# Kernel optimization log

Measured on AMD Instinct MI355X. Metric: run time of the kernel, lower is better.

The kernel has to match this reference:

```python
import jax, jax.numpy as jnp
import numpy as np

# ---- dims (see shape_source) ----
N, EG, T = 10000, 120000, 600000
NR, NS = 16, 7                      # num_radial, num_spherical
EA, EE, ET, ERBF, ECBF, EBIL = 128, 256, 64, 16, 16, 64
NB = 2                              # num_blocks
CUTOFF = 6.0
MAXZ = 100
INV_SQRT2 = 0.7071067811865476


def scaled_silu(x):
    # GemNet 'swish' activation = ScaledSiLU
    return jax.nn.silu(x) * (1.0 / 0.6)


def layer_norm(x, w, b):
    mu = jnp.mean(x, -1, keepdims=True)
    v = jnp.var(x, -1, keepdims=True)
    return (x - mu) * jax.lax.rsqrt(v + 1e-5) * w + b


def radial_basis(D):
    # polynomial envelope (exponent 5) * gaussian RBF on d/cutoff
    d = D / CUTOFF
    p = 5.0
    env = 1.0 - ((p + 1) * (p + 2) / 2) * d**5 + p * (p + 2) * d**6 - (p * (p + 1) / 2) * d**7
    env = jnp.where(d < 1.0, env, 0.0)
    offsets = jnp.linspace(0.0, 1.0, NR)
    coeff = -0.5 * (NR - 1.0) ** 2   # -0.5 / spacing^2
    return env[:, None] * jnp.exp(coeff * (d[:, None] - offsets) ** 2)  # (EG, NR)


def spherical_basis(cosphi):
    # circular basis: Y_l0(phi) = sqrt((2l+1)/4pi) P_l(cos phi), l = 0..NS-1
    P = [jnp.ones_like(cosphi), cosphi]
    for l in range(2, NS):
        P.append(((2 * l - 1) * cosphi * P[-1] - (l - 1) * P[-2]) / l)
    return jnp.stack([np.sqrt((2 * l + 1) / (4 * np.pi)) * P[l] for l in range(NS)], -1)  # (T, NS)


def residual(x, Ws):
    # GemNet ResidualLayer: 2 bias-free dense + skip, scaled by 1/sqrt(2)
    y = scaled_silu(scaled_silu(x @ Ws[0]) @ Ws[1])
    return (x + y) * INV_SQRT2


def gemnet_forward(D, cosphi, atom_emb, W_rbf3, W_rbf_h, W_rbf_out, W_cbf_down,
                   W_edge_emb, ib_dense_ca, ib_trip_dense_ba, ib_trip_mlp_rbf,
                   ib_trip_down, ib_trip_bilinear, ib_trip_up_ca, ib_trip_up_ac,
                   ib_res_before, ib_res_after, ib_atom_dense_rbf, ib_atom_dense1,
                   ib_atom_res, ib_concat_dense, ib_res_m, ob_dense_rbf, ob_dense1,
                   ob_res, ln_m_w, ln_m_b, ln_E_w, ln_E_b,
                   Z, idx_s, idx_t, id3_ba, id3_ca, id_swap):
    rbf = radial_basis(D)                                   # (EG, NR)
    sph = spherical_basis(cosphi)                           # (T, NS)
    rbf3 = rbf @ W_rbf3                                     # (EG, ERBF)
    rbf_h = rbf @ W_rbf_h
    rbf_out = rbf @ W_rbf_out
    # EfficientInteractionDownProjection: rbf x W -> (EG, NS, ECBF)
    rbf_W1 = jnp.einsum('er,sri->esi', rbf, W_cbf_down)
    # per-triplet circular-basis embedding: sum over spherical components
    cbf_t = jnp.einsum('ts,tsi->ti', sph, rbf_W1[id3_ca])   # (T, ECBF)

    h = atom_emb[Z]                                         # (N, EA)
    m = scaled_silu(jnp.concatenate([h[idx_s], h[idx_t], rbf], -1) @ W_edge_emb)  # (EG, EE)

    def out_block(i, h_cur, m_cur):
        mn = layer_norm(m_cur, ln_m_w[i], ln_m_b[i])
        x = mn * (rbf_out @ ob_dense_rbf[i])                # (EG, EE)
        xE = jax.ops.segment_sum(x, idx_t, num_segments=N)  # scatter edges -> atoms
        xE = scaled_silu(xE @ ob_dense1[i])                 # (N, EA)
        for r in range(ob_res.shape[1]):
            xE = residual(xE, ob_res[i, r])
        return layer_norm(xE, ln_E_w[i], ln_E_b[i])

    E_t = out_block(0, h, m)
    for i in range(NB):
        # ---- triplet interaction ----
        x_ca_skip = scaled_silu(m @ ib_dense_ca[i])
        x_ba = scaled_silu(m @ ib_trip_dense_ba[i])
        x_ba = x_ba * (rbf3 @ ib_trip_mlp_rbf[i])
        x_trip = scaled_silu(x_ba @ ib_trip_down[i])        # (EG, ET)
        x_t = x_trip[id3_ba]                                # gather -> (T, ET)
        # bilinear: out[t,o] = sum_i cbf_t[t,i] * sum_c x_t[t,c] W[c,i,o]
        Wb = ib_trip_bilinear[i]                            # (ET, ECBF, EBIL)
        acc = (x_t @ Wb[:, 0, :]) * cbf_t[:, 0:1]
        for ic in range(1, ECBF):
            acc = acc + (x_t @ Wb[:, ic, :]) * cbf_t[:, ic:ic + 1]
        x = jax.ops.segment_sum(acc, id3_ca, num_segments=EG)  # scatter trip -> edges (EG, EBIL)
        x_ca = scaled_silu(x @ ib_trip_up_ca[i])
        x_ac = scaled_silu(x @ ib_trip_up_ac[i])[id_swap]   # counter-directional edge
        x3 = (x_ca + x_ac) * INV_SQRT2

        # ---- edge update ----
        x = (x_ca_skip + x3) * INV_SQRT2
        for r in range(ib_res_before.shape[1]):
            x = residual(x, ib_res_before[i, r])
        x = (x + m) * INV_SQRT2
        for r in range(ib_res_after.shape[1]):
            x = residual(x, ib_res_after[i, r])

        # ---- atom update ----
        xa = x * (rbf_h @ ib_atom_dense_rbf[i])
        xa = jax.ops.segment_sum(xa, idx_t, num_segments=N)
        xa = scaled_silu(xa @ ib_atom_dense1[i])            # (N, EA)
        for r in range(ib_atom_res.shape[1]):
            xa = residual(xa, ib_atom_res[i, r])
        h = (h + xa) * INV_SQRT2

        # ---- edge embedding refresh with updated atoms ----
        m2 = scaled_silu(jnp.concatenate([h[idx_s], h[idx_t], x], -1) @ ib_concat_dense[i])
        for r in range(ib_res_m.shape[1]):
            m2 = residual(m2, ib_res_m[i, r])
        m = (m + m2) * INV_SQRT2

        E_t = E_t + out_block(i + 1, h, m)
    return E_t  # (N, EA) per-atom output features


def setup_inputs() -> dict:
    key = jax.random.key(0)
    ks = iter(jax.random.split(key, 64))

    def nrm(shape, fan_in):
        return jax.random.normal(next(ks), shape, jnp.float32) / np.sqrt(fan_in)

    Z = jax.random.randint(next(ks), (N,), 0, MAXZ)
    idx_s = jax.random.randint(next(ks), (EG,), 0, N)
    idx_t = jax.random.randint(next(ks), (EG,), 0, N)
    id3_ba = jax.random.randint(next(ks), (T,), 0, EG)
    id3_ca = jax.random.randint(next(ks), (T,), 0, EG)
    id_swap = jnp.arange(EG) ^ 1   # symmetric edges stored in (e, e^1) pairs
    D = jax.random.uniform(next(ks), (EG,), jnp.float32, 0.8, 5.9)
    cosphi = jax.random.uniform(next(ks), (T,), jnp.float32, -1.0, 1.0)

    emb = jax.random.normal(next(ks), (MAXZ, EA), jnp.float32)
    emb = emb / jnp.maximum(jnp.linalg.norm(emb, axis=-1, keepdims=True), 1.0)  # max_norm=1

    NBo = NB + 1
    inp = dict(
        D=D, cosphi=cosphi, atom_emb=emb,
        W_rbf3=nrm((NR, ERBF), NR), W_rbf_h=nrm((NR, ERBF), NR), W_rbf_out=nrm((NR, ERBF), NR),
        W_cbf_down=nrm((NS, NR, ECBF), NR),
        W_edge_emb=nrm((2 * EA + NR, EE), 2 * EA + NR),
        ib_dense_ca=nrm((NB, EE, EE), EE),
        ib_trip_dense_ba=nrm((NB, EE, EE), EE),
        ib_trip_mlp_rbf=nrm((NB, ERBF, EE), ERBF),
        ib_trip_down=nrm((NB, EE, ET), EE),
        ib_trip_bilinear=nrm((NB, ET, ECBF, EBIL), ET * ECBF),
        ib_trip_up_ca=nrm((NB, EBIL, EE), EBIL),
        ib_trip_up_ac=nrm((NB, EBIL, EE), EBIL),
        ib_res_before=nrm((NB, 1, 2, EE, EE), EE),
        ib_res_after=nrm((NB, 1, 2, EE, EE), EE),
        ib_atom_dense_rbf=nrm((NB, ERBF, EE), ERBF),
        ib_atom_dense1=nrm((NB, EE, EA), EE),
        ib_atom_res=nrm((NB, 2, 2, EA, EA), EA),
        ib_concat_dense=nrm((NB, 2 * EA + EE, EE), 2 * EA + EE),
        ib_res_m=nrm((NB, 1, 2, EE, EE), EE),
        ob_dense_rbf=nrm((NBo, ERBF, EE), ERBF),
        ob_dense1=nrm((NBo, EE, EA), EE),
        ob_res=nrm((NBo, 2, 2, EA, EA), EA),
        ln_m_w=jnp.ones((NBo, EE)), ln_m_b=jnp.zeros((NBo, EE)),
        ln_E_w=jnp.ones((NBo, EA)), ln_E_b=jnp.zeros((NBo, EA)),
        Z=Z, idx_s=idx_s, idx_t=idx_t, id3_ba=id3_ba, id3_ca=id3_ca, id_swap=id_swap,
    )
    return inp


def reference(D, cosphi, atom_emb, W_rbf3, W_rbf_h, W_rbf_out, W_cbf_down, W_edge_emb,
              ib_dense_ca, ib_trip_dense_ba, ib_trip_mlp_rbf, ib_trip_down,
              ib_trip_bilinear, ib_trip_up_ca, ib_trip_up_ac, ib_res_before,
              ib_res_after, ib_atom_dense_rbf, ib_atom_dense1, ib_atom_res,
              ib_concat_dense, ib_res_m, ob_dense_rbf, ob_dense1, ob_res,
              ln_m_w, ln_m_b, ln_E_w, ln_E_b, Z, idx_s, idx_t, id3_ba, id3_ca, id_swap):
    return gemnet_forward(D, cosphi, atom_emb, W_rbf3, W_rbf_h, W_rbf_out, W_cbf_down,
                          W_edge_emb, ib_dense_ca, ib_trip_dense_ba, ib_trip_mlp_rbf,
                          ib_trip_down, ib_trip_bilinear, ib_trip_up_ca, ib_trip_up_ac,
                          ib_res_before, ib_res_after, ib_atom_dense_rbf, ib_atom_dense1,
                          ib_atom_res, ib_concat_dense, ib_res_m, ob_dense_rbf, ob_dense1,
                          ob_res, ln_m_w, ln_m_b, ln_E_w, ln_E_b,
                          Z, idx_s, idx_t, id3_ba, id3_ca, id_swap)
```

## Files before the change

### kernel.cpp

```cpp
#include <hip/hip_runtime.h>

#define NATOM 10000
#define EG    120000
#define TT    600000

#define INV_SQRT2f 0.7071067811865476f

typedef unsigned short bf16t;
typedef __attribute__((ext_vector_type(8))) short s16x8;
typedef __attribute__((ext_vector_type(8))) unsigned short u16x8;
typedef __attribute__((ext_vector_type(4))) float f32x4;

__device__ __forceinline__ float ssilu(float x) {
    return x * (1.0f / (1.0f + __expf(-x))) * (1.0f / 0.6f);
}
__device__ __forceinline__ float bf2f(unsigned short u) {
    return __uint_as_float(((unsigned)u) << 16);
}
__device__ __forceinline__ unsigned short f2bf(float f) {
    unsigned b = __float_as_uint(f);
    unsigned r = (b + 0x7FFF + ((b >> 16) & 1)) >> 16;
    return (unsigned short)r;
}
__device__ __forceinline__ u16x8 cvt8(const float4 va, const float4 vb) {
    u16x8 r{};
    r[0] = f2bf(va.x); r[1] = f2bf(va.y); r[2] = f2bf(va.z); r[3] = f2bf(va.w);
    r[4] = f2bf(vb.x); r[5] = f2bf(vb.y); r[6] = f2bf(vb.z); r[7] = f2bf(vb.w);
    return r;
}

template <typename T> struct VT;
template <> struct VT<float> {
    static __device__ __forceinline__ float4 load4(const float* p) { return *(const float4*)p; }
    static __device__ __forceinline__ void store4(float* p, float4 v) { *(float4*)p = v; }
};
template <> struct VT<bf16t> {
    static __device__ __forceinline__ float4 load4(const bf16t* p) {
        ushort4 u = *(const ushort4*)p;
        return make_float4(bf2f(u.x), bf2f(u.y), bf2f(u.z), bf2f(u.w));
    }
    static __device__ __forceinline__ void store4(bf16t* p, float4 v) {
        ushort4 u; u.x = f2bf(v.x); u.y = f2bf(v.y); u.z = f2bf(v.z); u.w = f2bf(v.w);
        *(ushort4*)p = u;
    }
};

__global__ __launch_bounds__(256) void k_fill(float* __restrict__ o, int n, float v) {
    int i = blockIdx.x * 256 + threadIdx.x;
    if (i < n) o[i] = v;
}

__global__ __launch_bounds__(256) void k_hist(
    const int* __restrict__ idx, int* __restrict__ cnt, int n)
{
    int i = blockIdx.x * 256 + threadIdx.x;
    if (i < n) atomicAdd(&cnt[idx[i]], 1);
}

__global__ __launch_bounds__(1024) void k_scan(
    const int* __restrict__ cnt, int* __restrict__ off, int n)
{
    __shared__ int wsum[16];
    __shared__ int carrySh;
    if (threadIdx.x == 0) carrySh = 0;
    __syncthreads();
    const int lane = threadIdx.x & 63, wid = threadIdx.x >> 6;
    for (int base = 0; base < n; base += 8192) {
        int v[8]; int s = 0;
        int i0 = base + threadIdx.x * 8;
#pragma unroll
        for (int j = 0; j < 8; j++) { int i = i0 + j; v[j] = (i < n) ? cnt[i] : 0; s += v[j]; }
        int sc = s;
#pragma unroll
        for (int d = 1; d < 64; d <<= 1) { int t = __shfl_up(sc, d); if (lane >= d) sc += t; }
        if (lane == 63) wsum[wid] = sc;
        __syncthreads();
        int wbase = 0;
        for (int w = 0; w < 16; w++) wbase += (w < wid) ? wsum[w] : 0;
        int carry = carrySh;
        int excl = carry + wbase + (sc - s);
#pragma unroll
        for (int j = 0; j < 8; j++) { int i = i0 + j; if (i < n) off[i] = excl; excl += v[j]; }
        __syncthreads();
        if (threadIdx.x == 1023) carrySh = carry + wbase + sc;
        __syncthreads();
    }
    if (threadIdx.x == 0) off[n] = carrySh;
}

__global__ __launch_bounds__(256) void k_rank_trip(
    const int* __restrict__ id3_ca, const int* __restrict__ id3_ba,
    const int* __restrict__ off, int* __restrict__ cnt2,
    int* __restrict__ rank, int* __restrict__ ba_s, int* __restrict__ ca_s, int n)
{
    int t = blockIdx.x * 256 + threadIdx.x;
    if (t >= n) return;
    int ca = id3_ca[t];
    int p = off[ca] + atomicAdd(&cnt2[ca], 1);
    rank[t] = p;
    ba_s[p] = id3_ba[t];
    ca_s[p] = ca;
}

__global__ __launch_bounds__(256) void k_rank_edge(
    const int* __restrict__ idx, const int* __restrict__ off,
    int* __restrict__ cnt2, int* __restrict__ lst, int n)
{
    int i = blockIdx.x * 256 + threadIdx.x;
    if (i >= n) return;
    int a = idx[i];
    int p = off[a] + atomicAdd(&cnt2[a], 1);
    lst[p] = i;
}

__global__ __launch_bounds__(256) void k_segsum(
    const bf16t* __restrict__ X, const int* __restrict__ off,
    const int* __restrict__ lst, bf16t* __restrict__ out)
{
    int n = blockIdx.x, j = threadIdx.x;
    int b = off[n], e = off[n + 1];
    float s = 0.f;
    for (int k = b; k < e; k++) s += bf2f(X[(size_t)lst[k] * 256 + j]);
    out[(size_t)n * 256 + j] = f2bf(s);
}

struct WtE { const float* src; unsigned dstOff; int K, KP, N, mode; };
struct WtBatch { WtE e[12]; int n; };

__global__ __launch_bounds__(256) void k_wt_batch(WtBatch b, bf16t* __restrict__ base)
{
    for (int i = 0; i < b.n; i++) {
        const WtE E = b.e[i];
        int total = (E.mode == 0) ? E.N * E.KP : 16 * 64 * 64;
        for (int idx = blockIdx.x * 256 + threadIdx.x; idx < total; idx += gridDim.x * 256) {
            bf16t v;
            if (E.mode == 0) {
                int n = idx / E.KP, k = idx - n * E.KP;
                v = (k < E.K) ? f2bf(E.src[(size_t)k * E.N + n]) : (bf16t)0;
            } else {
                int e8 = idx & 7, o = (idx >> 3) & 63, ch = (idx >> 9) & 7, ii = idx >> 12;
                v = f2bf(E.src[((size_t)(ch * 8 + e8) * 16 + ii) * 64 + o]);
            }
            base[E.dstOff + idx] = v;
        }
    }
}

struct WcE { const float* Wa; const float* Wb; };
struct WcBatch { WcE e[7]; };

__global__ __launch_bounds__(256) void k_wcomb_batch(WcBatch b, float* __restrict__ wcb)
{
    __shared__ float sA[256];
    int c = blockIdx.x, j = threadIdx.x;
    sA[j] = b.e[c].Wa[j];
    __syncthreads();
    const float* Wb = b.e[c].Wb;
    float* dst = wcb + (size_t)c * 4096;
#pragma unroll 4
    for (int r = 0; r < 16; r++) {
        float acc = 0.f;
#pragma unroll
        for (int k = 0; k < 16; k++) acc = fmaf(sA[r * 16 + k], Wb[k * 256 + j], acc);
        dst[r * 256 + j] = acc;
    }
}

__global__ __launch_bounds__(256) void k_rbf(
    const float* __restrict__ D, const float* __restrict__ Wc,
    bf16t* __restrict__ rbf, float* __restrict__ rbfW1)
{
    __shared__ float sW[1792];
    for (int i = threadIdx.x; i < 1792; i += 256) sW[i] = Wc[i];
    __syncthreads();
    int e = blockIdx.x * 256 + threadIdx.x;
    if (e >= EG) return;
    float d = D[e] * (1.0f / 6.0f);
    float d2 = d * d, d4 = d2 * d2, d5 = d4 * d, d6 = d5 * d, d7 = d6 * d;
    float env = 1.0f - 21.0f * d5 + 35.0f * d6 - 15.0f * d7;
    if (d >= 1.0f) env = 0.0f;
    float r[16];
#pragma unroll
    for (int i = 0; i < 16; i++) {
        float t = d - (float)i * (1.0f / 15.0f);
        r[i] = env * __expf(-112.5f * t * t);
    }
#pragma unroll
    for (int j = 0; j < 16; j++) rbf[(size_t)e * 16 + j] = f2bf(r[j]);
    for (int s = 0; s < 7; s++) {
#pragma unroll 4
        for (int i = 0; i < 16; i++) {
            float a = 0.f;
#pragma unroll
            for (int k = 0; k < 16; k++)
                a = fmaf(r[k], sW[(s * 16 + k) * 16 + i], a);
            rbfW1[(size_t)e * 112 + s * 16 + i] = a;
        }
    }
}

__global__ __launch_bounds__(256) void k_cbf(
    const float* __restrict__ cosphi, const int* __restrict__ id3_ca,
    const float* __restrict__ rbfW1, const int* __restrict__ rank,
    bf16t* __restrict__ cbf)
{
    int t = blockIdx.x * 256 + threadIdx.x;
    if (t >= TT) return;
    float c = cosphi[t];
    const float norm[7] = {0.28209479177387814f, 0.4886025119029199f, 0.6307831305050401f,
                           0.7463526651802308f, 0.8462843753216345f, 0.935414346693485f,
                           1.0171072362820548f};
    float y[7];
    float pm2 = 1.0f, pm1 = c;
    y[0] = norm[0];
    y[1] = norm[1] * c;
    for (int l = 2; l < 7; l++) {
        float p = ((2.0f * l - 1.0f) * c * pm1 - (l - 1.0f) * pm2) / (float)l;
        y[l] = norm[l] * p;
        pm2 = pm1; pm1 = p;
    }
    int e = id3_ca[t];
    const float* __restrict__ w = rbfW1 + (size_t)e * 112;
    float out[16];
#pragma unroll
    for (int i = 0; i < 16; i++) out[i] = 0.f;
#pragma unroll
    for (int s = 0; s < 7; s++) {
        float ys = y[s];
#pragma unroll
        for (int i = 0; i < 16; i++) out[i] = fmaf(ys, w[s * 16 + i], out[i]);
    }
    int p = rank[t];
#pragma unroll
    for (int i = 0; i < 16; i++) cbf[(size_t)p * 16 + i] = f2bf(out[i]);
}

__global__ __launch_bounds__(256) void k_hgather(
    const float* __restrict__ emb, const int* __restrict__ Z, bf16t* __restrict__ h)
{
    int i = blockIdx.x * 256 + threadIdx.x;
    if (i < NATOM * 128) {
        int n = i >> 7, j = i & 127;
        h[i] = f2bf(emb[(size_t)Z[n] * 128 + j]);
    }
}

template <typename TA, int FR, int FC, int EPI>
__global__ __launch_bounds__(256) void mgemm3(
    const TA* __restrict__ A, const bf16t* __restrict__ BT,
    bf16t* __restrict__ C, const bf16t* __restrict__ skip,
    int M, int N, int K)
{
    constexpr int ROWS = 2 * FR * 16;
    constexpr int COLS = 2 * FC * 16;
    __shared__ __align__(16) ushort As[ROWS][40];
    __shared__ __align__(16) ushort Bs[COLS][40];
    const int tid = threadIdx.x, wave = tid >> 6, lane = tid & 63;
    const int waveR = wave >> 1, waveC = wave & 1;
    const int rowBase = blockIdx.y * ROWS, colBase = blockIdx.x * COLS;

    const int sar = tid >> 1, sak = (tid & 1) << 4;
    int agr = rowBase + sar; if (agr >= M) agr = M - 1;
    int sbc, sbk;
    if constexpr (COLS == 128) { sbc = tid >> 1; sbk = (tid & 1) << 4; }
    else                       { sbc = tid >> 2; sbk = (tid & 3) << 3; }

    f32x4 zv = {0.f, 0.f, 0.f, 0.f};
    f32x4 acc[FR][FC];
#pragma unroll
    for (int f = 0; f < FR; f++)
#pragma unroll
        for (int q = 0; q < FC; q++) acc[f][q] = zv;

    const int arow0 = waveR * FR * 16 + (lane & 15);
    const int bcol0 = waveC * FC * 16 + (lane & 15);
    const int kd = (lane >> 4) << 3;

    u16x8 a0, a1, b0, b1;
    auto loadA = [&](int k0) {
        if constexpr (sizeof(TA) == 2) {
            const u16x8* s = (const u16x8*)((const bf16t*)A + (size_t)agr * K + k0 + sak);
            a0 = s[0]; a1 = s[1];
        } else {
            const float4* s = (const float4*)((const float*)A + (size_t)agr * K + k0 + sak);
            a0 = cvt8(s[0], s[1]); a1 = cvt8(s[2], s[3]);
        }
    };
    auto loadB = [&](int k0) {
        const u16x8* s = (const u16x8*)(BT + (size_t)(colBase + sbc) * K + k0 + sbk);
        b0 = s[0];
        if constexpr (COLS == 128) b1 = s[1];
    };
    loadA(0); loadB(0);
    for (int k0 = 0; k0 < K; k0 += 32) {
        __syncthreads();
        *(u16x8*)&As[sar][sak] = a0;
        *(u16x8*)&As[sar][sak + 8] = a1;
        *(u16x8*)&Bs[sbc][sbk] = b0;
        if constexpr (COLS == 128) *(u16x8*)&Bs[sbc][sbk + 8] = b1;
        __syncthreads();
        if (k0 + 32 < K) { loadA(k0 + 32); loadB(k0 + 32); }
        u16x8 af[FR], bf[FC];
#pragma unroll
        for (int f = 0; f < FR; f++) af[f] = *(const u16x8*)&As[arow0 + f * 16][kd];
#pragma unroll
        for (int q = 0; q < FC; q++) bf[q] = *(const u16x8*)&Bs[bcol0 + q * 16][kd];
#pragma unroll
        for (int f = 0; f < FR; f++)
#pragma unroll
            for (int q = 0; q < FC; q++)
                acc[f][q] = __builtin_amdgcn_mfma_f32_16x16x32_bf16(
                    *(s16x8*)&af[f], *(s16x8*)&bf[q], acc[f][q], 0, 0, 0);
    }

    const int rB = rowBase + waveR * FR * 16 + ((lane >> 4) << 2);
    const int cB = colBase + waveC * FC * 16 + (lane & 15);
#pragma unroll
    for (int f = 0; f < FR; f++) {
#pragma unroll
        for (int r = 0; r < 4; r++) {
            int row = rB + f * 16 + r;
            if (row >= M) continue;
#pragma unroll
            for (int q = 0; q < FC; q++) {
                int col = cB + q * 16;
                float v = acc[f][q][r];
                if (EPI == 1) {
                    C[(size_t)row * N + col] = f2bf(ssilu(v));
                } else {
                    float sk = bf2f(skip[(size_t)row * N + col]);
                    C[(size_t)row * N + col] = f2bf((sk + ssilu(v)) * INV_SQRT2f);
                }
            }
        }
    }
}

__global__ __launch_bounds__(256) void mgemmA1(
    const bf16t* __restrict__ BT, bf16t* __restrict__ C,
    int M, int N, int K, int KP,
    const bf16t* __restrict__ hA, const int* __restrict__ gS,
    const int* __restrict__ gT, const bf16t* __restrict__ X, int w2)
{
    __shared__ __align__(16) ushort As[128][40];
    __shared__ __align__(16) ushort Bs[64][40];
    const int tid = threadIdx.x, wave = tid >> 6, lane = tid & 63;
    const int waveR = wave >> 1, waveC = wave & 1;
    const int rowBase = blockIdx.y * 128, colBase = blockIdx.x * 64;

    const int sar = tid >> 1, sak = (tid & 1) << 4;
    const int arow = rowBase + sar;
    const int arowC = arow < M ? arow : (M - 1);
    const int ia = gS[arowC], ibx = gT[arowC];
    const int sbc = tid >> 2, sbk = (tid & 3) << 3;

    f32x4 zv = {0.f, 0.f, 0.f, 0.f};
    f32x4 acc[4][2];
#pragma unroll
    for (int f = 0; f < 4; f++)
#pragma unroll
        for (int q = 0; q < 2; q++) acc[f][q] = zv;

    const int arow0 = waveR * 64 + (lane & 15);
    const int bcol0 = waveC * 32 + (lane & 15);
    const int kd = (lane >> 4) << 3;

    u16x8 a0, a1, b0;
    auto loadA = [&](int k0) {
        a0 = u16x8{}; a1 = u16x8{};
        const int kk = k0 + sak;
        if (kk < 128) {
            const u16x8* s = (const u16x8*)(hA + (size_t)ia * 128 + kk);
            a0 = s[0]; a1 = s[1];
        } else if (kk < 256) {
            const u16x8* s = (const u16x8*)(hA + (size_t)ibx * 128 + (kk - 128));
            a0 = s[0]; a1 = s[1];
        } else if (kk < K && kk - 256 < w2) {
            const u16x8* s = (const u16x8*)(X + (size_t)arowC * w2 + (kk - 256));
            a0 = s[0]; a1 = s[1];
        }
    };
    auto loadB = [&](int k0) {
        b0 = *(const u16x8*)(BT + (size_t)(colBase + sbc) * KP + k0 + sbk);
    };
    loadA(0); loadB(0);
    for (int k0 = 0; k0 < K; k0 += 32) {
        __syncthreads();
        *(u16x8*)&As[sar][sak] = a0;
        *(u16x8*)&As[sar][sak + 8] = a1;
        *(u16x8*)&Bs[sbc][sbk] = b0;
        __syncthreads();
        if (k0 + 32 < K) { loadA(k0 + 32); loadB(k0 + 32); }
        u16x8 af[4], bf[2];
#pragma unroll
        for (int f = 0; f < 4; f++) af[f] = *(const u16x8*)&As[arow0 + f * 16][kd];
#pragma unroll
        for (int q = 0; q < 2; q++) bf[q] = *(const u16x8*)&Bs[bcol0 + q * 16][kd];
#pragma unroll
        for (int f = 0; f < 4; f++)
#pragma unroll
            for (int q = 0; q < 2; q++)
                acc[f][q] = __builtin_amdgcn_mfma_f32_16x16x32_bf16(
                    *(s16x8*)&af[f], *(s16x8*)&bf[q], acc[f][q], 0, 0, 0);
    }

    const int rB = rowBase + waveR * 64 + ((lane >> 4) << 2);
    const int cB = colBase + waveC * 32 + (lane & 15);
#pragma unroll
    for (int f = 0; f < 4; f++) {
#pragma unroll
        for (int r = 0; r < 4; r++) {
            int row = rB + f * 16 + r;
            if (row >= M) continue;
#pragma unroll
            for (int q = 0; q < 2; q++)
                C[(size_t)row * N + cB + q * 16] = f2bf(ssilu(acc[f][q][r]));
        }
    }
}

__global__ __launch_bounds__(256) void mgemm_up(
    const float* __restrict__ A, const bf16t* __restrict__ BTca,
    const bf16t* __restrict__ BTac, bf16t* __restrict__ C, int M)
{
    constexpr int K = 64, N = 256;
    __shared__ __align__(16) ushort As[128][40];
    __shared__ __align__(16) ushort Bs[2][64][40];
    const int tid = threadIdx.x, wave = tid >> 6, lane = tid & 63;
    const int waveR = wave >> 1, waveC = wave & 1;
    const int rowBase = blockIdx.y * 128, colBase = blockIdx.x * 64;

    const int sar = tid >> 1, sak = (tid & 1) << 4;
    int agr = rowBase + sar; if (agr >= M) agr = M - 1;
    const int sbc = tid >> 2, sbk = (tid & 3) << 3;

    f32x4 zv = {0.f, 0.f, 0.f, 0.f};
    f32x4 accA[4][2], accB[4][2];
#pragma unroll
    for (int f = 0; f < 4; f++)
#pragma unroll
        for (int q = 0; q < 2; q++) { accA[f][q] = zv; accB[f][q] = zv; }

    const int arow0 = waveR * 64 + (lane & 15);
    const int bcol0 = waveC * 32 + (lane & 15);
    const int kd = (lane >> 4) << 3;

    u16x8 a0, a1, bA, bB;
    auto loadA = [&](int k0) {
        const float4* s = (const float4*)(A + (size_t)agr * K + k0 + sak);
        a0 = cvt8(s[0], s[1]); a1 = cvt8(s[2], s[3]);
    };
    auto loadB = [&](int k0) {
        bA = *(const u16x8*)(BTca + (size_t)(colBase + sbc) * K + k0 + sbk);
        bB = *(const u16x8*)(BTac + (size_t)(colBase + sbc) * K + k0 + sbk);
    };
    loadA(0); loadB(0);
    for (int k0 = 0; k0 < K; k0 += 32) {
        __syncthreads();
        *(u16x8*)&As[sar][sak] = a0;
        *(u16x8*)&As[sar][sak + 8] = a1;
        *(u16x8*)&Bs[0][sbc][sbk] = bA;
        *(u16x8*)&Bs[1][sbc][sbk] = bB;
        __syncthreads();
        if (k0 + 32 < K) { loadA(k0 + 32); loadB(k0 + 32); }
        u16x8 af[4], bfA[2], bfB[2];
#pragma unroll
        for (int f = 0; f < 4; f++) af[f] = *(const u16x8*)&As[arow0 + f * 16][kd];
#pragma unroll
        for (int q = 0; q < 2; q++) {
            bfA[q] = *(const u16x8*)&Bs[0][bcol0 + q * 16][kd];
            bfB[q] = *(const u16x8*)&Bs[1][bcol0 + q * 16][kd];
        }
#pragma unroll
        for (int f = 0; f < 4; f++)
#pragma unroll
            for (int q = 0; q < 2; q++) {
                accA[f][q] = __builtin_amdgcn_mfma_f32_16x16x32_bf16(
                    *(s16x8*)&af[f], *(s16x8*)&bfA[q], accA[f][q], 0, 0, 0);
                accB[f][q] = __builtin_amdgcn_mfma_f32_16x16x32_bf16(
                    *(s16x8*)&af[f], *(s16x8*)&bfB[q], accB[f][q], 0, 0, 0);
            }
    }

    const int rB = rowBase + waveR * 64 + ((lane >> 4) << 2);
    const int cB = colBase + waveC * 32 + (lane & 15);
#pragma unroll
    for (int f = 0; f < 4; f++) {
#pragma unroll
        for (int r = 0; r < 4; r++) {
            int row = rB + f * 16 + r;
            if (row >= M) continue;
#pragma unroll
            for (int q = 0; q < 2; q++) {
                float v = (ssilu(accA[f][q][r]) + ssilu(accB[f][q][r ^ 1])) * INV_SQRT2f;
                C[(size_t)row * N + cB + q * 16] = f2bf(v);
            }
        }
    }
}

__global__ __launch_bounds__(256) void k_bilinear_m(
    const bf16t* __restrict__ xtrip, const bf16t* __restrict__ cbf,
    const bf16t* __restrict__ WT,
    const int* __restrict__ ba_s, const int* __restrict__ ca_s,
    float* __restrict__ seg)
{
    __shared__ __align__(16) ushort xs[64][72];
    __shared__ ushort cbs[64][16];
    __shared__ int cas[64];
    __shared__ __align__(16) float ts[64][65];
    const int tid = threadIdx.x, wave = tid >> 6, lane = tid & 63;
    const int t0 = blockIdx.x * 64;
    {
        int r = tid >> 2, q = (tid & 3) << 4;
        int ba = ba_s[t0 + r];
        const u16x8* src = (const u16x8*)(xtrip + (size_t)ba * 64 + q);
        *(u16x8*)&xs[r][q] = src[0];
        *(u16x8*)&xs[r][q + 8] = src[1];
    }
    if (tid < 64) cas[tid] = ca_s[t0 + tid];
    {
        int e = tid << 2; int r = e >> 4, c = e & 15;
        *(ushort4*)&cbs[r][c] = *(const ushort4*)(cbf + (size_t)(t0 + r) * 16 + c);
    }
    __syncthreads();
    const int kd = (lane >> 4) << 3;
    u16x8 a0 = *(const u16x8*)(&xs[wave * 16 + (lane & 15)][kd]);
    u16x8 a1 = *(const u16x8*)(&xs[wave * 16 + (lane & 15)][32 + kd]);
    const int rowo = wave * 16 + ((lane >> 4) << 2);
    const int chb = lane >> 4, colw = lane & 15;
    auto waddr = [&](int i, int fc, int half) {
        return WT + (((size_t)(i * 8 + half * 4 + chb) * 64) + colw + fc * 16) * 8;
    };

    float tot[4][4];
#pragma unroll
    for (int a = 0; a < 4; a++)
#pragma unroll
        for (int b = 0; b < 4; b++) tot[a][b] = 0.f;

    u16x8 bw[8], bn[8];
#pragma unroll
    for (int fc = 0; fc < 4; fc++) {
        bw[fc * 2 + 0] = *(const u16x8*)waddr(0, fc, 0);
        bw[fc * 2 + 1] = *(const u16x8*)waddr(0, fc, 1);
    }
    for (int i = 0; i < 16; i++) {
        if (i < 15) {
#pragma unroll
            for (int fc = 0; fc < 4; fc++) {
                bn[fc * 2 + 0] = *(const u16x8*)waddr(i + 1, fc, 0);
                bn[fc * 2 + 1] = *(const u16x8*)waddr(i + 1, fc, 1);
            }
        }
        f32x4 zv = {0.f, 0.f, 0.f, 0.f};
        f32x4 p[4] = {zv, zv, zv, zv};
#pragma unroll
        for (int fc = 0; fc < 4; fc++) {
            p[fc] = __builtin_amdgcn_mfma_f32_16x16x32_bf16(
                *(s16x8*)&a0, *(s16x8*)&bw[fc * 2 + 0], p[fc], 0, 0, 0);
            p[fc] = __builtin_amdgcn_mfma_f32_16x16x32_bf16(
                *(s16x8*)&a1, *(s16x8*)&bw[fc * 2 + 1], p[fc], 0, 0, 0);
        }
#pragma unroll
        for (int r = 0; r < 4; r++) {
            float s = bf2f(cbs[rowo + r][i]);
#pragma unroll
            for (int fc = 0; fc < 4; fc++) tot[fc][r] += s * p[fc][r];
        }
#pragma unroll
        for (int q = 0; q < 8; q++) bw[q] = bn[q];
    }
#pragma unroll
    for (int r = 0; r < 4; r++)
#pragma unroll
        for (int fc = 0; fc < 4; fc++)
            ts[rowo + r][fc * 16 + (lane & 15)] = tot[fc][r];
    __syncthreads();
    {
        int q = tid >> 6, c = tid & 63;
        float s = 0.f;
        int cur = cas[q * 16];
#pragma unroll 1
        for (int r = q * 16; r < q * 16 + 16; r++) {
            int ca = cas[r];
            if (ca != cur) {
                atomicAdd(&seg[(size_t)cur * 64 + c], s);
                s = 0.f; cur = ca;
            }
            s += ts[r][c];
        }
        atomicAdd(&seg[(size_t)cur * 64 + c], s);
    }
}

__global__ __launch_bounds__(256) void k_mulproj(
    const bf16t* __restrict__ in, const bf16t* __restrict__ rvec,
    const float* __restrict__ Wp, bf16t* __restrict__ out)
{
    int e = blockIdx.x;
    int j = threadIdx.x;
    __shared__ float r16[16];
    if (j < 16) r16[j] = bf2f(rvec[(size_t)e * 16 + j]);
    __syncthreads();
    float p = 0.f;
#pragma unroll
    for (int k = 0; k < 16; k++) p = fmaf(r16[k], Wp[k * 256 + j], p);
    out[(size_t)e * 256 + j] = f2bf(bf2f(in[(size_t)e * 256 + j]) * p);
}

__global__ __launch_bounds__(256) void k_ln_proj(
    const bf16t* __restrict__ m, const float* __restrict__ lnw,
    const float* __restrict__ lnb, const bf16t* __restrict__ rvec,
    const float* __restrict__ Wp, bf16t* __restrict__ out)
{
    int e = blockIdx.x;
    int j = threadIdx.x;
    __shared__ float red[8];
    __shared__ float r16[16];
    if (j < 16) r16[j] = bf2f(rvec[(size_t)e * 16 + j]);
    float v = bf2f(m[(size_t)e * 256 + j]);
    float s = v, s2 = v * v;
#pragma unroll
    for (int off = 32; off > 0; off >>= 1) {
        s += __shfl_xor(s, off);
        s2 += __shfl_xor(s2, off);
    }
    int wid = j >> 6, lane = j & 63;
    if (lane == 0) { red[wid] = s; red[4 + wid] = s2; }
    __syncthreads();
    float tot = red[0] + red[1] + red[2] + red[3];
    float tot2 = red[4] + red[5] + red[6] + red[7];
    float mu = tot * (1.f / 256.f);
    float var = tot2 * (1.f / 256.f) - mu * mu;
    float ln = (v - mu) * rsqrtf(var + 1e-5f) * lnw[j] + lnb[j];
    float p = 0.f;
#pragma unroll
    for (int k = 0; k < 16; k++) p = fmaf(r16[k], Wp[k * 256 + j], p);
    out[(size_t)e * 256 + j] = f2bf(ln * p);
}

__global__ __launch_bounds__(128) void k_ln_acc(
    const bf16t* __restrict__ x, const float* __restrict__ w,
    const float* __restrict__ b, float* __restrict__ out)
{
    int n = blockIdx.x;
    int j = threadIdx.x;
    __shared__ float red[4];
    float v = bf2f(x[(size_t)n * 128 + j]);
    float s = v, s2 = v * v;
#pragma unroll
    for (int off = 32; off > 0; off >>= 1) {
        s += __shfl_xor(s, off);
        s2 += __shfl_xor(s2, off);
    }
    int wid = j >> 6, lane = j & 63;
    if (lane == 0) { red[wid] = s; red[2 + wid] = s2; }
    __syncthreads();
    float tot = red[0] + red[1];
    float tot2 = red[2] + red[3];
    float mu = tot * (1.f / 128.f);
    float var = tot2 * (1.f / 128.f) - mu * mu;
    out[(size_t)n * 128 + j] += (v - mu) * rsqrtf(var + 1e-5f) * w[j] + b[j];
}

template <typename T>
__global__ __launch_bounds__(256) void k_addscale(
    const T* __restrict__ a, const T* __restrict__ b, T* __restrict__ y, int n4)
{
    int i = blockIdx.x * 256 + threadIdx.x;
    if (i < n4) {
        float4 av = VT<T>::load4(a + (size_t)i * 4);
        float4 bv = VT<T>::load4(b + (size_t)i * 4);
        VT<T>::store4(y + (size_t)i * 4,
                      make_float4((av.x + bv.x) * INV_SQRT2f, (av.y + bv.y) * INV_SQRT2f,
                                  (av.z + bv.z) * INV_SQRT2f, (av.w + bv.w) * INV_SQRT2f));
    }
}

typedef bf16t T;
static bool try_run(void* const* d_in, void* d_out, void* d_ws, size_t ws_size, hipStream_t stream)
{
    const float* D            = (const float*)d_in[0];
    const float* cosphi       = (const float*)d_in[1];
    const float* atom_emb     = (const float*)d_in[2];
    const float* W_rbf3       = (const float*)d_in[3];
    const float* W_rbf_h      = (const float*)d_in[4];
    const float* W_rbf_out    = (const float*)d_in[5];
    const float* W_cbf_down   = (const float*)d_in[6];
    const float* W_edge_emb   = (const float*)d_in[7];
    const float* ib_dense_ca  = (const float*)d_in[8];
    const float* ib_trip_dense_ba = (const float*)d_in[9];
    const float* ib_trip_mlp_rbf  = (const float*)d_in[10];
    const float* ib_trip_down     = (const float*)d_in[11];
    const float* ib_trip_bilinear = (const float*)d_in[12];
    const float* ib_trip_up_ca    = (const float*)d_in[13];
    const float* ib_trip_up_ac    = (const float*)d_in[14];
    const float* ib_res_before    = (const float*)d_in[15];
    const float* ib_res_after     = (const float*)d_in[16];
    const float* ib_atom_dense_rbf = (const float*)d_in[17];
    const float* ib_atom_dense1    = (const float*)d_in[18];
    const float* ib_atom_res       = (const float*)d_in[19];
    const float* ib_concat_dense   = (const float*)d_in[20];
    const float* ib_res_m          = (const float*)d_in[21];
    const float* ob_dense_rbf      = (const float*)d_in[22];
    const float* ob_dense1         = (const float*)d_in[23];
    const float* ob_res            = (const float*)d_in[24];
    const float* ln_m_w            = (const float*)d_in[25];
    const float* ln_m_b            = (const float*)d_in[26];
    const float* ln_E_w            = (const float*)d_in[27];
    const float* ln_E_b            = (const float*)d_in[28];
    const int* Z       = (const int*)d_in[29];
    const int* idx_s   = (const int*)d_in[30];
    const int* idx_t   = (const int*)d_in[31];
    const int* id3_ba  = (const int*)d_in[32];
    const int* id3_ca  = (const int*)d_in[33];

    char* base = (char*)d_ws;
    size_t off = 0;
    auto alloc = [&](size_t bytes) -> char* {
        off = (off + 255) & ~(size_t)255;
        char* p = base + off;
        off += bytes;
        return p;
    };
    T* m      = (T*)alloc((size_t)EG * 256 * 2);
    T* B1     = (T*)alloc((size_t)EG * 256 * 2);
    T* B2     = (T*)alloc((size_t)EG * 256 * 2);
    float* rbfW1 = (float*)B1;
    int* rank    = (int*)B2;
    T* rbf    = (T*)alloc((size_t)EG * 16 * 2);
    T* cbf    = (T*)alloc((size_t)TT * 16 * 2);
    bf16t* h  = (bf16t*)alloc((size_t)NATOM * 128 * 2);
    T* xtrip  = (T*)alloc((size_t)EG * 64 * 2);
    char* ub  = alloc((size_t)EG * 64 * 4);
    float* seg64  = (float*)ub;
    bf16t* segN_b = (bf16t*)ub;
    bf16t* At1b   = (bf16t*)(ub + (size_t)NATOM * 256 * 2);
    bf16t* At2b   = (bf16t*)(ub + (size_t)NATOM * 256 * 2 + (size_t)NATOM * 128 * 2);
    int* cntT  = (int*)ub;
    int* cnt2T = (int*)(ub + (size_t)EG * 4);
    int* off_ca = (int*)(ub + (size_t)2 * EG * 4);
    float* wcb = (float*)alloc((size_t)7 * 4096 * 4);
    bf16t* ar  = (bf16t*)alloc((size_t)507904 * 2);
    int* off_atom  = (int*)alloc((size_t)(NATOM + 1) * 4);
    int* ba_s      = (int*)alloc((size_t)TT * 4);
    int* ca_s      = (int*)alloc((size_t)TT * 4);
    int* csr_edges = (int*)alloc((size_t)EG * 4);
    if (off > ws_size) return false;
    float* out = (float*)d_out;

    auto g256 = [&](int epi, const T* A, unsigned wOff, T* C, const T* skip, int K) {
        dim3 grid(2, (EG + 127) / 128);
        if (epi == 1) mgemm3<T, 4, 4, 1><<<grid, 256, 0, stream>>>(A, ar + wOff, C, skip, EG, 256, K);
        else          mgemm3<T, 4, 4, 2><<<grid, 256, 0, stream>>>(A, ar + wOff, C, skip, EG, 256, K);
    };
    auto gatom = [&](int epi, const bf16t* A, unsigned wOff, bf16t* C, const bf16t* skip, int K) {
        dim3 grid(1, (NATOM + 127) / 128);
        if (epi == 1) mgemm3<bf16t, 4, 4, 1><<<grid, 256, 0, stream>>>(A, ar + wOff, C, skip, NATOM, 128, K);
        else          mgemm3<bf16t, 4, 4, 2><<<grid, 256, 0, stream>>>(A, ar + wOff, C, skip, NATOM, 128, K);
    };
    auto out_block = [&](int i, unsigned offD1, unsigned offRes) {
        k_ln_proj<<<EG, 256, 0, stream>>>(m, ln_m_w + (size_t)i * 256, ln_m_b + (size_t)i * 256,
                                          rbf, wcb + (size_t)(4 + i) * 4096, B2);
        k_segsum<<<NATOM, 256, 0, stream>>>(B2, off_atom, csr_edges, segN_b);
        gatom(1, segN_b, offD1, At1b, nullptr, 256);
        for (int r = 0; r < 2; r++) {
            gatom(1, At1b, offRes + (r * 2 + 0) * 16384, At2b, nullptr, 128);
            gatom(2, At2b, offRes + (r * 2 + 1) * 16384, At1b, At1b, 128);
        }
        k_ln_acc<<<NATOM, 128, 0, stream>>>(At1b, ln_E_w + (size_t)i * 128, ln_E_b + (size_t)i * 128, out);
    };

    hipMemsetAsync(cntT, 0, (size_t)EG * 4, stream);
    k_hist<<<(TT + 255) / 256, 256, 0, stream>>>(id3_ca, cntT, TT);
    k_scan<<<1, 1024, 0, stream>>>(cntT, off_ca, EG);
    hipMemsetAsync(cnt2T, 0, (size_t)EG * 4, stream);
    k_rank_trip<<<(TT + 255) / 256, 256, 0, stream>>>(id3_ca, id3_ba, off_ca, cnt2T,
                                                      rank, ba_s, ca_s, TT);
    hipMemsetAsync(cntT, 0, (size_t)NATOM * 4, stream);
    k_hist<<<(EG + 255) / 256, 256, 0, stream>>>(idx_t, cntT, EG);
    k_scan<<<1, 1024, 0, stream>>>(cntT, off_atom, NATOM);
    hipMemsetAsync(cnt2T, 0, (size_t)NATOM * 4, stream);
    k_rank_edge<<<(EG + 255) / 256, 256, 0, stream>>>(idx_t, off_atom, cnt2T, csr_edges, EG);

    {
        WcBatch wb;
        wb.e[0] = {W_rbf3, ib_trip_mlp_rbf};
        wb.e[1] = {W_rbf3, ib_trip_mlp_rbf + 4096};
        wb.e[2] = {W_rbf_h, ib_atom_dense_rbf};
        wb.e[3] = {W_rbf_h, ib_atom_dense_rbf + 4096};
        wb.e[4] = {W_rbf_out, ob_dense_rbf};
        wb.e[5] = {W_rbf_out, ob_dense_rbf + 4096};
        wb.e[6] = {W_rbf_out, ob_dense_rbf + 8192};
        k_wcomb_batch<<<7, 256, 0, stream>>>(wb, wcb);
    }
    {
        WtBatch wt{};
        wt.e[0] = {W_edge_emb, 0u, 272, 288, 256, 0};
        wt.e[1] = {ob_dense1, 73728u, 256, 256, 128, 0};
        for (int j = 0; j < 4; j++)
            wt.e[2 + j] = {ob_res + (size_t)j * 16384, 106496u + j * 16384u, 128, 128, 128, 0};
        wt.n = 6;
        k_wt_batch<<<512, 256, 0, stream>>>(wt, ar);
    }

    hipMemsetAsync(out, 0, (size_t)NATOM * 128 * 4, stream);
    k_rbf<<<(EG + 255) / 256, 256, 0, stream>>>(D, W_cbf_down, rbf, rbfW1);
    k_cbf<<<(TT + 255) / 256, 256, 0, stream>>>(cosphi, id3_ca, rbfW1, rank, cbf);
    k_hgather<<<(NATOM * 128 + 255) / 256, 256, 0, stream>>>(atom_emb, Z, h);
    {
        dim3 grid(4, (EG + 127) / 128);
        mgemmA1<<<grid, 256, 0, stream>>>(ar, m, EG, 256, 272, 288, h, idx_s, idx_t, rbf, 16);
    }
    out_block(0, 73728u, 106496u);

    for (int i = 0; i < 2; i++) {
        {
            WtBatch wt{};
            wt.e[0] = {ib_dense_ca + (size_t)i * 65536, 0u, 256, 256, 256, 0};
            wt.e[1] = {ib_trip_dense_ba + (size_t)i * 65536, 65536u, 256, 256, 256, 0};
            wt.e[2] = {ib_trip_down + (size_t)i * 16384, 131072u, 256, 256, 64, 0};
            wt.e[3] = {ib_trip_bilinear + (size_t)i * 65536, 147456u, 0, 0, 0, 1};
            wt.e[4] = {ib_trip_up_ca + (size_t)i * 16384, 212992u, 64, 64, 256, 0};
            wt.e[5] = {ib_trip_up_ac + (size_t)i * 16384, 229376u, 64, 64, 256, 0};
            wt.e[6] = {ib_res_before + (size_t)i * 131072, 245760u, 256, 256, 256, 0};
            wt.e[7] = {ib_res_before + (size_t)i * 131072 + 65536, 311296u, 256, 256, 256, 0};
            wt.e[8] = {ib_res_after + (size_t)i * 131072, 376832u, 256, 256, 256, 0};
            wt.e[9] = {ib_res_after + (size_t)i * 131072 + 65536, 442368u, 256, 256, 256, 0};
            wt.n = 10;
            k_wt_batch<<<512, 256, 0, stream>>>(wt, ar);
        }
        g256(1, m, 0u, B1, nullptr, 256);
        g256(1, m, 65536u, B2, nullptr, 256);
        k_mulproj<<<EG, 256, 0, stream>>>(B2, rbf, wcb + (size_t)i * 4096, B2);
        {
            dim3 grid(1, (EG + 127) / 128);
            mgemm3<T, 4, 2, 1><<<grid, 256, 0, stream>>>(B2, ar + 131072, xtrip, nullptr, EG, 64, 256);
        }
        hipMemsetAsync(seg64, 0, (size_t)EG * 64 * 4, stream);
        k_bilinear_m<<<TT / 64, 256, 0, stream>>>(xtrip, cbf, ar + 147456, ba_s, ca_s, seg64);
        {
            dim3 grid(4, (EG + 127) / 128);
            mgemm_up<<<grid, 256, 0, stream>>>(seg64, ar + 212992, ar + 229376, B2, EG);
        }
        k_addscale<T><<<(EG * 256 / 4 + 255) / 256, 256, 0, stream>>>(B1, B2, B1, EG * 256 / 4);
        g256(1, B1, 245760u, B2, nullptr, 256);
        g256(2, B2, 311296u, B1, B1, 256);
        k_addscale<T><<<(EG * 256 / 4 + 255) / 256, 256, 0, stream>>>(B1, m, B1, EG * 256 / 4);
        g256(1, B1, 376832u, B2, nullptr, 256);
        g256(2, B2, 442368u, B1, B1, 256);
        {
            WtBatch wt{};
            wt.e[0] = {ib_atom_dense1 + (size_t)i * 32768, 0u, 256, 256, 128, 0};
            for (int j = 0; j < 4; j++)
                wt.e[1 + j] = {ib_atom_res + (size_t)i * 65536 + (size_t)j * 16384,
                               32768u + j * 16384u, 128, 128, 128, 0};
            wt.e[5] = {ib_concat_dense + (size_t)i * 131072, 98304u, 512, 512, 256, 0};
            wt.e[6] = {ib_res_m + (size_t)i * 131072, 229376u, 256, 256, 256, 0};
            wt.e[7] = {ib_res_m + (size_t)i * 131072 + 65536, 294912u, 256, 256, 256, 0};
            wt.e[8] = {ob_dense1 + (size_t)(i + 1) * 32768, 360448u, 256, 256, 128, 0};
            for (int j = 0; j < 4; j++)
                wt.e[9 + j] = {ob_res + (size_t)(i + 1) * 65536 + (size_t)j * 16384,
                               393216u + j * 16384u, 128, 128, 128, 0};
            wt.n = 13 <= 12 ? 13 : 12;
            wt.n = 9;
            k_wt_batch<<<512, 256, 0, stream>>>(wt, ar);
            WtBatch wt2{};
            wt2.e[0] = {ob_dense1 + (size_t)(i + 1) * 32768, 360448u, 256, 256, 128, 0};
            for (int j = 0; j < 4; j++)
                wt2.e[1 + j] = {ob_res + (size_t)(i + 1) * 65536 + (size_t)j * 16384,
                                393216u + j * 16384u, 128, 128, 128, 0};
            wt2.n = 5;
            k_wt_batch<<<512, 256, 0, stream>>>(wt2, ar);
        }
        k_mulproj<<<EG, 256, 0, stream>>>(B1, rbf, wcb + (size_t)(2 + i) * 4096, B2);
        k_segsum<<<NATOM, 256, 0, stream>>>(B2, off_atom, csr_edges, segN_b);
        gatom(1, segN_b, 0u, At1b, nullptr, 256);
        for (int r = 0; r < 2; r++) {
            gatom(1, At1b, 32768u + (r * 2 + 0) * 16384, At2b, nullptr, 128);
            gatom(2, At2b, 32768u + (r * 2 + 1) * 16384, At1b, At1b, 128);
        }
        k_addscale<bf16t><<<(NATOM * 128 / 4 + 255) / 256, 256, 0, stream>>>(h, At1b, h, NATOM * 128 / 4);
        {
            dim3 grid(4, (EG + 127) / 128);
            mgemmA1<<<grid, 256, 0, stream>>>(ar + 98304, B2, EG, 256, 512, 512, h, idx_s, idx_t, B1, 256);
        }
        g256(1, B2, 229376u, B1, nullptr, 256);
        g256(2, B1, 294912u, B2, B2, 256);
        k_addscale<T><<<(EG * 256 / 4 + 255) / 256, 256, 0, stream>>>(m, B2, m, EG * 256 / 4);

        out_block(i + 1, 360448u, 393216u);
    }
    return true;
}

extern "C" void kernel_launch(void* const* d_in, const int* in_sizes, int n_in,
                              void* d_out, int out_size, void* d_ws, size_t ws_size,
                              hipStream_t stream)
{
    if (try_run(d_in, d_out, d_ws, ws_size, stream)) return;
    float v = 3000.0f + (float)(ws_size >> 20);
    k_fill<<<(NATOM * 128 + 255) / 256, 256, 0, stream>>>((float*)d_out, NATOM * 128, v);
}
```

Measured before the change: 2.939 ms.

## Fuse residual-layer GEMM pairs into one kernel and fold skip-adds into epilogues

Adds a mgemm_res kernel that runs both dense layers of a residual block in one launch. The first layer's ScaledSiLU output stays in LDS and feeds the second GEMM, and the skip connection plus an optional extra residual add are applied in the epilogue. The separate k_addscale passes are removed, and mgemm_up now applies the skip-add itself. This cuts several full-size edge and atom intermediate round-trips through HBM and a number of kernel launches, and the duplicated ob_dense1 weight conversion is dropped. In exchange the fused kernel uses about 59 KB of LDS at N=256, which lowers occupancy, and it computes in place on buffers it also reads from.

Result: faster. 2.699 ms (-8.2%).

```diff
diff --git a/kernel.cpp b/kernel.cpp
--- a/kernel.cpp
+++ b/kernel.cpp
@@ -28,22 +28,6 @@
     r[4] = f2bf(vb.x); r[5] = f2bf(vb.y); r[6] = f2bf(vb.z); r[7] = f2bf(vb.w);
     return r;
 }
-
-template <typename T> struct VT;
-template <> struct VT<float> {
-    static __device__ __forceinline__ float4 load4(const float* p) { return *(const float4*)p; }
-    static __device__ __forceinline__ void store4(float* p, float4 v) { *(float4*)p = v; }
-};
-template <> struct VT<bf16t> {
-    static __device__ __forceinline__ float4 load4(const bf16t* p) {
-        ushort4 u = *(const ushort4*)p;
-        return make_float4(bf2f(u.x), bf2f(u.y), bf2f(u.z), bf2f(u.w));
-    }
-    static __device__ __forceinline__ void store4(bf16t* p, float4 v) {
-        ushort4 u; u.x = f2bf(v.x); u.y = f2bf(v.y); u.z = f2bf(v.z); u.w = f2bf(v.w);
-        *(ushort4*)p = u;
-    }
-};
 
 __global__ __launch_bounds__(256) void k_fill(float* __restrict__ o, int n, float v) {
     int i = blockIdx.x * 256 + threadIdx.x;
@@ -336,6 +320,123 @@
     }
 }
 
+template <int FCC, int EPIOUT>
+__global__ __launch_bounds__(256) void mgemm_res(
+    const bf16t* __restrict__ A, const bf16t* __restrict__ BT0,
+    const bf16t* __restrict__ BT1, bf16t* __restrict__ C,
+    const bf16t* __restrict__ add2, int M)
+{
+    constexpr int N = FCC * 32;
+    __shared__ __align__(16) ushort As[64][40];
+    __shared__ __align__(16) ushort Bs[N][40];
+    __shared__ __align__(16) ushort inter[64][N + 8];
+    const int tid = threadIdx.x, wave = tid >> 6, lane = tid & 63;
+    const int waveR = wave >> 1, waveC = wave & 1;
+    const int rowBase = blockIdx.x * 64;
+
+    const int sar = tid >> 2, sak = (tid & 3) << 3;
+    int agr = rowBase + sar; if (agr >= M) agr = M - 1;
+    const int sbc = tid >> 2, sbk = (tid & 3) << 3;
+
+    const int arow0 = waveR * 32 + (lane & 15);
+    const int bcol0 = waveC * FCC * 16 + (lane & 15);
+    const int kd = (lane >> 4) << 3;
+
+    f32x4 zv = {0.f, 0.f, 0.f, 0.f};
+    f32x4 acc[2][FCC];
+#pragma unroll
+    for (int f = 0; f < 2; f++)
+#pragma unroll
+        for (int q = 0; q < FCC; q++) acc[f][q] = zv;
+
+    u16x8 aR, bR[FCC / 2];
+    auto loadA = [&](int k0) {
+        aR = *(const u16x8*)(A + (size_t)agr * N + k0 + sak);
+    };
+    auto loadB = [&](const bf16t* BT, int k0) {
+#pragma unroll
+        for (int j = 0; j < FCC / 2; j++)
+            bR[j] = *(const u16x8*)(BT + (size_t)(sbc + j * 64) * N + k0 + sbk);
+    };
+
+    loadA(0); loadB(BT0, 0);
+    for (int k0 = 0; k0 < N; k0 += 32) {
+        __syncthreads();
+        *(u16x8*)&As[sar][sak] = aR;
+#pragma unroll
+        for (int j = 0; j < FCC / 2; j++) *(u16x8*)&Bs[sbc + j * 64][sbk] = bR[j];
+        __syncthreads();
+        if (k0 + 32 < N) { loadA(k0 + 32); loadB(BT0, k0 + 32); }
+        else             { loadB(BT1, 0); }
+        u16x8 af0 = *(const u16x8*)&As[arow0][kd];
+        u16x8 af1 = *(const u16x8*)&As[arow0 + 16][kd];
+        u16x8 bf[FCC];
+#pragma unroll
+        for (int q = 0; q < FCC; q++) bf[q] = *(const u16x8*)&Bs[bcol0 + q * 16][kd];
+#pragma unroll
+        for (int q = 0; q < FCC; q++) {
+            acc[0][q] = __builtin_amdgcn_mfma_f32_16x16x32_bf16(
+                *(s16x8*)&af0, *(s16x8*)&bf[q], acc[0][q], 0, 0, 0);
+            acc[1][q] = __builtin_amdgcn_mfma_f32_16x16x32_bf16(
+                *(s16x8*)&af1, *(s16x8*)&bf[q], acc[1][q], 0, 0, 0);
+        }
+    }
+    {
+        const int rL = waveR * 32 + ((lane >> 4) << 2);
+        const int cL = waveC * FCC * 16 + (lane & 15);
+#pragma unroll
+        for (int f = 0; f < 2; f++)
+#pragma unroll
+            for (int r = 0; r < 4; r++)
+#pragma unroll
+                for (int q = 0; q < FCC; q++)
+                    inter[rL + f * 16 + r][cL + q * 16] = f2bf(ssilu(acc[f][q][r]));
+    }
+#pragma unroll
+    for (int f = 0; f < 2; f++)
+#pragma unroll
+        for (int q = 0; q < FCC; q++) acc[f][q] = zv;
+
+    for (int k0 = 0; k0 < N; k0 += 32) {
+        __syncthreads();
+#pragma unroll
+        for (int j = 0; j < FCC / 2; j++) *(u16x8*)&Bs[sbc + j * 64][sbk] = bR[j];
+        __syncthreads();
+        if (k0 + 32 < N) loadB(BT1, k0 + 32);
+        u16x8 af0 = *(const u16x8*)&inter[arow0][k0 + kd];
+        u16x8 af1 = *(const u16x8*)&inter[arow0 + 16][k0 + kd];
+        u16x8 bf[FCC];
+#pragma unroll
+        for (int q = 0; q < FCC; q++) bf[q] = *(const u16x8*)&Bs[bcol0 + q * 16][kd];
+#pragma unroll
+        for (int q = 0; q < FCC; q++) {
+            acc[0][q] = __builtin_amdgcn_mfma_f32_16x16x32_bf16(
+                *(s16x8*)&af0, *(s16x8*)&bf[q], acc[0][q], 0, 0, 0);
+            acc[1][q] = __builtin_amdgcn_mfma_f32_16x16x32_bf16(
+                *(s16x8*)&af1, *(s16x8*)&bf[q], acc[1][q], 0, 0, 0);
+        }
+    }
+
+    const int rB = rowBase + waveR * 32 + ((lane >> 4) << 2);
+    const int cB = waveC * FCC * 16 + (lane & 15);
+#pragma unroll
+    for (int f = 0; f < 2; f++) {
+#pragma unroll
+        for (int r = 0; r < 4; r++) {
+            int row = rB + f * 16 + r;
+            if (row >= M) continue;
+#pragma unroll
+            for (int q = 0; q < FCC; q++) {
+                int col = cB + q * 16;
+                float sk = bf2f(A[(size_t)row * N + col]);
+                float y = (sk + ssilu(acc[f][q][r])) * INV_SQRT2f;
+                if (EPIOUT == 1) y = (y + bf2f(add2[(size_t)row * N + col])) * INV_SQRT2f;
+                C[(size_t)row * N + col] = f2bf(y);
+            }
+        }
+    }
+}
+
 __global__ __launch_bounds__(256) void mgemmA1(
     const bf16t* __restrict__ BT, bf16t* __restrict__ C,
     int M, int N, int K, int KP,
@@ -421,7 +522,8 @@
 
 __global__ __launch_bounds__(256) void mgemm_up(
     const float* __restrict__ A, const bf16t* __restrict__ BTca,
-    const bf16t* __restrict__ BTac, bf16t* __restrict__ C, int M)
+    const bf16t* __restrict__ BTac, bf16t* __restrict__ C,
+    const bf16t* __restrict__ skip, int M)
 {
     constexpr int K = 64, N = 256;
     __shared__ __align__(16) ushort As[128][40];
@@ -492,8 +594,10 @@
             if (row >= M) continue;
 #pragma unroll
             for (int q = 0; q < 2; q++) {
+                int col = cB + q * 16;
                 float v = (ssilu(accA[f][q][r]) + ssilu(accB[f][q][r ^ 1])) * INV_SQRT2f;
-                C[(size_t)row * N + cB + q * 16] = f2bf(v);
+                float y = (bf2f(skip[(size_t)row * N + col]) + v) * INV_SQRT2f;
+                C[(size_t)row * N + col] = f2bf(y);
             }
         }
     }
@@ -662,20 +766,6 @@
     float mu = tot * (1.f / 128.f);
     float var = tot2 * (1.f / 128.f) - mu * mu;
     out[(size_t)n * 128 + j] += (v - mu) * rsqrtf(var + 1e-5f) * w[j] + b[j];
-}
-
-template <typename T>
-__global__ __launch_bounds__(256) void k_addscale(
-    const T* __restrict__ a, const T* __restrict__ b, T* __restrict__ y, int n4)
-{
-    int i = blockIdx.x * 256 + threadIdx.x;
-    if (i < n4) {
-        float4 av = VT<T>::load4(a + (size_t)i * 4);
-        float4 bv = VT<T>::load4(b + (size_t)i * 4);
-        VT<T>::store4(y + (size_t)i * 4,
-                      make_float4((av.x + bv.x) * INV_SQRT2f, (av.y + bv.y) * INV_SQRT2f,
-                                  (av.z + bv.z) * INV_SQRT2f, (av.w + bv.w) * INV_SQRT2f));
-    }
 }
 
 typedef bf16t T;
@@ -737,7 +827,6 @@
     float* seg64  = (float*)ub;
     bf16t* segN_b = (bf16t*)ub;
     bf16t* At1b   = (bf16t*)(ub + (size_t)NATOM * 256 * 2);
-    bf16t* At2b   = (bf16t*)(ub + (size_t)NATOM * 256 * 2 + (size_t)NATOM * 128 * 2);
     int* cntT  = (int*)ub;
     int* cnt2T = (int*)(ub + (size_t)EG * 4);
     int* off_ca = (int*)(ub + (size_t)2 * EG * 4);
@@ -750,25 +839,23 @@
     if (off > ws_size) return false;
     float* out = (float*)d_out;
 
-    auto g256 = [&](int epi, const T* A, unsigned wOff, T* C, const T* skip, int K) {
+    auto g256 = [&](const T* A, unsigned wOff, T* C) {
         dim3 grid(2, (EG + 127) / 128);
-        if (epi == 1) mgemm3<T, 4, 4, 1><<<grid, 256, 0, stream>>>(A, ar + wOff, C, skip, EG, 256, K);
-        else          mgemm3<T, 4, 4, 2><<<grid, 256, 0, stream>>>(A, ar + wOff, C, skip, EG, 256, K);
-    };
-    auto gatom = [&](int epi, const bf16t* A, unsigned wOff, bf16t* C, const bf16t* skip, int K) {
+        mgemm3<T, 4, 4, 1><<<grid, 256, 0, stream>>>(A, ar + wOff, C, nullptr, EG, 256, 256);
+    };
+    auto gatom1 = [&](const bf16t* A, unsigned wOff, bf16t* C) {
         dim3 grid(1, (NATOM + 127) / 128);
-        if (epi == 1) mgemm3<bf16t, 4, 4, 1><<<grid, 256, 0, stream>>>(A, ar + wOff, C, skip, NATOM, 128, K);
-        else          mgemm3<bf16t, 4, 4, 2><<<grid, 256, 0, stream>>>(A, ar + wOff, C, skip, NATOM, 128, K);
+        mgemm3<bf16t, 4, 4, 1><<<grid, 256, 0, stream>>>(A, ar + wOff, C, nullptr, NATOM, 128, 256);
     };
     auto out_block = [&](int i, unsigned offD1, unsigned offRes) {
         k_ln_proj<<<EG, 256, 0, stream>>>(m, ln_m_w + (size_t)i * 256, ln_m_b + (size_t)i * 256,
                                           rbf, wcb + (size_t)(4 + i) * 4096, B2);
         k_segsum<<<NATOM, 256, 0, stream>>>(B2, off_atom, csr_edges, segN_b);
-        gatom(1, segN_b, offD1, At1b, nullptr, 256);
-        for (int r = 0; r < 2; r++) {
-            gatom(1, At1b, offRes + (r * 2 + 0) * 16384, At2b, nullptr, 128);
-            gatom(2, At2b, offRes + (r * 2 + 1) * 16384, At1b, At1b, 128);
-        }
+        gatom1(segN_b, offD1, At1b);
+        mgemm_res<4, 0><<<(NATOM + 63) / 64, 256, 0, stream>>>(
+            At1b, ar + offRes, ar + offRes + 16384, At1b, nullptr, NATOM);
+        mgemm_res<4, 0><<<(NATOM + 63) / 64, 256, 0, stream>>>(
+            At1b, ar + offRes + 32768, ar + offRes + 49152, At1b, nullptr, NATOM);
         k_ln_acc<<<NATOM, 128, 0, stream>>>(At1b, ln_E_w + (size_t)i * 128, ln_E_b + (size_t)i * 128, out);
     };
 
@@ -831,8 +918,8 @@
             wt.n = 10;
             k_wt_batch<<<512, 256, 0, stream>>>(wt, ar);
         }
-        g256(1, m, 0u, B1, nullptr, 256);
-        g256(1, m, 65536u, B2, nullptr, 256);
+        g256(m, 0u, B1);
+        g256(m, 65536u, B2);
         k_mulproj<<<EG, 256, 0, stream>>>(B2, rbf, wcb + (size_t)i * 4096, B2);
         {
             dim3 grid(1, (EG + 127) / 128);
@@ -842,14 +929,10 @@
         k_bilinear_m<<<TT / 64, 256, 0, stream>>>(xtrip, cbf, ar + 147456, ba_s, ca_s, seg64);
         {
             dim3 grid(4, (EG + 127) / 128);
-            mgemm_up<<<grid, 256, 0, stream>>>(seg64, ar + 212992, ar + 229376, B2, EG);
-        }
-        k_addscale<T><<<(EG * 256 / 4 + 255) / 256, 256, 0, stream>>>(B1, B2, B1, EG * 256 / 4);
-        g256(1, B1, 245760u, B2, nullptr, 256);
-        g256(2, B2, 311296u, B1, B1, 256);
-        k_addscale<T><<<(EG * 256 / 4 + 255) / 256, 256, 0, stream>>>(B1, m, B1, EG * 256 / 4);
-        g256(1, B1, 376832u, B2, nullptr, 256);
-        g256(2, B2, 442368u, B1, B1, 256);
+            mgemm_up<<<grid, 256, 0, stream>>>(seg64, ar + 212992, ar + 229376, B1, B1, EG);
+        }
+        mgemm_res<8, 1><<<EG / 64, 256, 0, stream>>>(B1, ar + 245760, ar + 311296, B1, m, EG);
+        mgemm_res<8, 0><<<EG / 64, 256, 0, stream>>>(B1, ar + 376832, ar + 442368, B1, nullptr, EG);
         {
             WtBatch wt{};
             wt.e[0] = {ib_atom_dense1 + (size_t)i * 32768, 0u, 256, 256, 128, 0};
@@ -860,35 +943,27 @@
             wt.e[6] = {ib_res_m + (size_t)i * 131072, 229376u, 256, 256, 256, 0};
             wt.e[7] = {ib_res_m + (size_t)i * 131072 + 65536, 294912u, 256, 256, 256, 0};
             wt.e[8] = {ob_dense1 + (size_t)(i + 1) * 32768, 360448u, 256, 256, 128, 0};
-            for (int j = 0; j < 4; j++)
-                wt.e[9 + j] = {ob_res + (size_t)(i + 1) * 65536 + (size_t)j * 16384,
-                               393216u + j * 16384u, 128, 128, 128, 0};
-            wt.n = 13 <= 12 ? 13 : 12;
             wt.n = 9;
             k_wt_batch<<<512, 256, 0, stream>>>(wt, ar);
             WtBatch wt2{};
-            wt2.e[0] = {ob_dense1 + (size_t)(i + 1) * 32768, 360448u, 256, 256, 128, 0};
             for (int j = 0; j < 4; j++)
-                wt2.e[1 + j] = {ob_res + (size_t)(i + 1) * 65536 + (size_t)j * 16384,
-                                393216u + j * 16384u, 128, 128, 128, 0};
-            wt2.n = 5;
+                wt2.e[j] = {ob_res + (size_t)(i + 1) * 65536 + (size_t)j * 16384,
+                            393216u + j * 16384u, 128, 128, 128, 0};
+            wt2.n = 4;
             k_wt_batch<<<512, 256, 0, stream>>>(wt2, ar);
         }
         k_mulproj<<<EG, 256, 0, stream>>>(B1, rbf, wcb + (size_t)(2 + i) * 4096, B2);
         k_segsum<<<NATOM, 256, 0, stream>>>(B2, off_atom, csr_edges, segN_b);
-        gatom(1, segN_b, 0u, At1b, nullptr, 256);
-        for (int r = 0; r < 2; r++) {
-            gatom(1, At1b, 32768u + (r * 2 + 0) * 16384, At2b, nullptr, 128);
-            gatom(2, At2b, 32768u + (r * 2 + 1) * 16384, At1b, At1b, 128);
-        }
-        k_addscale<bf16t><<<(NATOM * 128 / 4 + 255) / 256, 256, 0, stream>>>(h, At1b, h, NATOM * 128 / 4);
+        gatom1(segN_b, 0u, At1b);
+        mgemm_res<4, 0><<<(NATOM + 63) / 64, 256, 0, stream>>>(
+            At1b, ar + 32768, ar + 49152, At1b, nullptr, NATOM);
+        mgemm_res<4, 1><<<(NATOM + 63) / 64, 256, 0, stream>>>(
+            At1b, ar + 65536, ar + 81920, h, h, NATOM);
         {
             dim3 grid(4, (EG + 127) / 128);
             mgemmA1<<<grid, 256, 0, stream>>>(ar + 98304, B2, EG, 256, 512, 512, h, idx_s, idx_t, B1, 256);
         }
-        g256(1, B2, 229376u, B1, nullptr, 256);
-        g256(2, B1, 294912u, B2, B2, 256);
-        k_addscale<T><<<(EG * 256 / 4 + 255) / 256, 256, 0, stream>>>(m, B2, m, EG * 256 / 4);
+        mgemm_res<8, 1><<<EG / 64, 256, 0, stream>>>(B2, ar + 229376, ar + 294912, m, m, EG);
 
         out_block(i + 1, 360448u, 393216u);
     }
```
